# Kernel tuning notes

Measured on AMD Instinct MI355X. Metric: run time of the kernel, lower is better.

Reference implementation:

```python
import math
import jax, jax.numpy as jnp
import numpy as np

H = 256      # hidden_size
HEADS = 8
DK = H // HEADS
B = 32
DL = 290     # drug length
PL = 1000    # protein length


def _pe(length, d):
    # sinusoidal positional encoding, d even
    pos = jnp.arange(length, dtype=jnp.float32)[:, None]
    div = jnp.exp(jnp.arange(0, d, 2, dtype=jnp.float32) * (-math.log(10000.0) / d))
    ang = pos * div  # [L, d/2]
    pe = jnp.zeros((length, d), jnp.float32)
    pe = pe.at[:, 0::2].set(jnp.sin(ang)).at[:, 1::2].set(jnp.cos(ang))
    return pe


def setup_inputs() -> dict:
    key = jax.random.key(0)
    ks = iter(jax.random.split(key, 48))
    def lin(din, dout):
        return jax.random.normal(next(ks), (din, dout), jnp.float32) * 0.02, jnp.zeros((dout,), jnp.float32)
    inp = {}
    inp['drug'] = jax.random.normal(next(ks), (B, DL, H), jnp.float32)
    inp['protein'] = jax.random.normal(next(ks), (B, PL, H), jnp.float32)
    inp['scale_d'] = jnp.ones((1,), jnp.float32)
    inp['scale_p'] = jnp.ones((1,), jnp.float32)
    for name in ['q_d', 'k_p', 'v_p', 'q_p', 'k_d', 'v_d', 'out_d', 'out_p']:
        w, b = lin(H, H)
        inp['w_' + name] = w
        inp['b_' + name] = b
    inp['alpha'] = jnp.asarray(0.5, jnp.float32)
    for name in ['fc_dp', 'fc_pd']:
        w, b = lin(HEADS, H)
        inp['w_' + name] = w
        inp['b_' + name] = b
    for name in ['gd', 'gp']:
        w, b = lin(H, H)
        inp['w_' + name] = w
        inp['b_' + name] = b
    return inp


def _split_heads(x):
    b, l, _ = x.shape
    return x.reshape(b, l, HEADS, DK).transpose(0, 2, 1, 3)  # [b, h, l, dk]


def _forward(drug, protein, scale_d, scale_p,
             w_q_d, b_q_d, w_k_p, b_k_p, w_v_p, b_v_p,
             w_q_p, b_q_p, w_k_d, b_k_d, w_v_d, b_v_d,
             alpha, w_out_d, b_out_d, w_out_p, b_out_p,
             w_fc_dp, b_fc_dp, w_fc_pd, b_fc_pd,
             w_gd, b_gd, w_gp, b_gp):
    b, dl, h = drug.shape
    pl = protein.shape[1]
    # positional encoding (buffers, non-learned except scale)
    drug_e = drug + scale_d * _pe(dl, h)
    prot_e = protein + scale_p * _pe(pl, h)

    Qd = _split_heads(drug_e @ w_q_d + b_q_d)   # [b,h,dl,dk]
    Kp = _split_heads(prot_e @ w_k_p + b_k_p)   # [b,h,pl,dk]
    Vp = _split_heads(prot_e @ w_v_p + b_v_p)
    Qp = _split_heads(prot_e @ w_q_p + b_q_p)
    Kd = _split_heads(drug_e @ w_k_d + b_k_d)
    Vd = _split_heads(drug_e @ w_v_d + b_v_d)

    inv_sqrt = 1.0 / math.sqrt(DK)
    attn_dp = jnp.einsum('bhid,bhjd->bhij', Qd, Kp) * inv_sqrt      # [b,h,dl,pl]
    # (Q_p K_d^T)^T along last two dims -> [b,h,dl,pl]
    attn_pd = jnp.einsum('bhjd,bhid->bhij', Qp, Kd) * inv_sqrt
    a = jax.nn.sigmoid(alpha)
    A = jax.nn.softmax(a * attn_dp + (1.0 - a) * attn_pd, axis=-1)  # [b,h,dl,pl]

    ctx_d = jnp.einsum('bhij,bhjd->bhid', A, Vp)  # [b,h,dl,dk]
    ctx_p = jnp.einsum('bhij,bhid->bhjd', A, Vd)  # [b,h,pl,dk]
    ctx_d = ctx_d.transpose(0, 2, 1, 3).reshape(b, dl, h) @ w_out_d + b_out_d
    ctx_p = ctx_p.transpose(0, 2, 1, 3).reshape(b, pl, h) @ w_out_p + b_out_p

    attn_dp_m = jnp.mean(A, axis=-1).transpose(0, 2, 1)   # [b,dl,heads]
    drug_attn = attn_dp_m @ w_fc_dp + b_fc_dp             # [b,dl,h]
    attn_pd_m = jnp.mean(A, axis=-2).transpose(0, 2, 1)   # [b,pl,heads]
    prot_attn = attn_pd_m @ w_fc_pd + b_fc_pd             # [b,pl,h]

    drug_gate = jax.nn.sigmoid(drug_e @ w_gd + b_gd)
    prot_gate = jax.nn.sigmoid(prot_e @ w_gp + b_gp)
    ctx_d = ctx_d * drug_gate
    ctx_p = ctx_p * prot_gate

    drug_upd = drug_e + ctx_d * jax.nn.sigmoid(drug_attn)
    prot_upd = prot_e + ctx_p * jax.nn.sigmoid(prot_attn)
    return jnp.concatenate([drug_upd, prot_upd], axis=1)  # [b, dl+pl, h]


def reference(drug, protein, scale_d, scale_p,
              w_q_d, b_q_d, w_k_p, b_k_p, w_v_p, b_v_p,
              w_q_p, b_q_p, w_k_d, b_k_d, w_v_d, b_v_d,
              alpha, w_out_d, b_out_d, w_out_p, b_out_p,
              w_fc_dp, b_fc_dp, w_fc_pd, b_fc_pd,
              w_gd, b_gd, w_gp, b_gp):
    return _forward(drug, protein, scale_d, scale_p,
                    w_q_d, b_q_d, w_k_p, b_k_p, w_v_p, b_v_p,
                    w_q_p, b_q_p, w_k_d, b_k_d, w_v_d, b_v_d,
                    alpha, w_out_d, b_out_d, w_out_p, b_out_p,
                    w_fc_dp, b_fc_dp, w_fc_pd, b_fc_pd,
                    w_gd, b_gd, w_gp, b_gp)
```

## Files before the change

kernel.cpp:

```cpp
#include <hip/hip_runtime.h>
#include <math.h>

typedef __attribute__((ext_vector_type(8))) short bf16x8;
typedef __attribute__((ext_vector_type(4))) float f32x4;
typedef unsigned short u16;
typedef unsigned int u32;

#define DEVFN static __device__ __forceinline__

constexpr int NB  = 32;
constexpr int DLn = 290;
constexpr int PLc = 1000;
constexpr int MD  = NB * DLn;
constexpr int MP  = NB * PLc;

DEVFN u16 f2b(float f) {
    u32 u = __builtin_bit_cast(u32, f);
    u32 r = u + 0x7fffu + ((u >> 16) & 1u);
    return (u16)(r >> 16);
}
DEVFN float b2f(u16 s) { return __builtin_bit_cast(float, (u32)s << 16); }
DEVFN float sigm(float x) { return 1.0f / (1.0f + __expf(-x)); }

__global__ void pe_kernel(float* __restrict__ pe) {
    int p = blockIdx.x, c = threadIdx.x;
    float div = __expf((float)(c & ~1) * (-9.210340371976184f / 256.0f));
    float ang = (float)p * div;
    pe[p * 256 + c] = (c & 1) ? cosf(ang) : sinf(ang);
}

__global__ void eadd_kernel(const float* __restrict__ drug, const float* __restrict__ prot,
                            const float* __restrict__ scale_d, const float* __restrict__ scale_p,
                            const float* __restrict__ pe,
                            u16* __restrict__ e_d, u16* __restrict__ e_p) {
    int r = blockIdx.x, c = threadIdx.x;
    if (r < MD) {
        int i = r % DLn;
        e_d[(size_t)r * 256 + c] = f2b(drug[(size_t)r * 256 + c] + scale_d[0] * pe[i * 256 + c]);
    } else {
        int rr = r - MD;
        int j = rr % PLc;
        e_p[(size_t)rr * 256 + c] = f2b(prot[(size_t)rr * 256 + c] + scale_p[0] * pe[j * 256 + c]);
    }
}

struct WPtrs { const float* w[10]; };
__global__ void wprep_kernel(WPtrs wp, u16* __restrict__ wt) {
    int m = blockIdx.x >> 8, n = blockIdx.x & 255, k = threadIdx.x;
    wt[((size_t)m << 16) + n * 256 + k] = f2b(wp.w[m][k * 256 + n]);
}

struct GCfg { const u16* A; const u16* BT; const float* bias; u16* C; int mtiles; int sig; };
struct GCfg8 { GCfg c[8]; };

__global__ __launch_bounds__(256) void gemm_kernel(GCfg8 cfgs) {
    const GCfg cfg = cfgs.c[blockIdx.z];
    const int mt = blockIdx.x;
    if (mt >= cfg.mtiles) return;
    const int nt = blockIdx.y;
    __shared__ u16 As[64][264];
    __shared__ u16 Bs[64][264];
    const int tid = threadIdx.x;
    const int lane = tid & 63, w = tid >> 6, ln = lane & 15, g = lane >> 4;
    const int lr = tid >> 2, lc = tid & 3;
    const u16* Ag = cfg.A + (size_t)(mt * 64 + lr) * 256 + lc * 8;
    const u16* Bg = cfg.BT + (size_t)(nt * 64 + lr) * 256 + lc * 8;
    uint4 av[8], bv[8];
    #pragma unroll
    for (int kk = 0; kk < 8; kk++) {
        av[kk] = *(const uint4*)(Ag + kk * 32);
        bv[kk] = *(const uint4*)(Bg + kk * 32);
    }
    #pragma unroll
    for (int kk = 0; kk < 8; kk++) {
        *(uint4*)&As[lr][lc * 8 + kk * 32] = av[kk];
        *(uint4*)&Bs[lr][lc * 8 + kk * 32] = bv[kk];
    }
    __syncthreads();
    const int m0 = (w >> 1) * 32, n0 = (w & 1) * 32;
    f32x4 acc[2][2] = {};
    #pragma unroll
    for (int k0 = 0; k0 < 8; k0++) {
        #pragma unroll
        for (int mi = 0; mi < 2; mi++) {
            bf16x8 af = *(const bf16x8*)&As[m0 + mi * 16 + ln][k0 * 32 + g * 8];
            #pragma unroll
            for (int ni = 0; ni < 2; ni++) {
                bf16x8 bfv = *(const bf16x8*)&Bs[n0 + ni * 16 + ln][k0 * 32 + g * 8];
                acc[mi][ni] = __builtin_amdgcn_mfma_f32_16x16x32_bf16(af, bfv, acc[mi][ni], 0, 0, 0);
            }
        }
    }
    #pragma unroll
    for (int mi = 0; mi < 2; mi++) {
        #pragma unroll
        for (int ni = 0; ni < 2; ni++) {
            const int n = nt * 64 + n0 + ni * 16 + ln;
            const float bb = cfg.bias[n];
            const int rowb = mt * 64 + m0 + mi * 16 + g * 4;
            #pragma unroll
            for (int r = 0; r < 4; r++) {
                float v = acc[mi][ni][r] + bb;
                if (cfg.sig) v = sigm(v);
                cfg.C[(size_t)(rowb + r) * 256 + n] = f2b(v);
            }
        }
    }
}

__global__ __launch_bounds__(512) void attn_kernel(
        const u16* __restrict__ Qd, const u16* __restrict__ Kd, const u16* __restrict__ Vd,
        const u16* __restrict__ Kp, const u16* __restrict__ Vp, const u16* __restrict__ Qp,
        const float* __restrict__ alpha,
        u16* __restrict__ ctx_d, u16* __restrict__ ctx_p, float* __restrict__ cm) {
    __shared__ u16 Ks[2][64][72];
    __shared__ union {
        struct { u16 VpT[2][32][72]; u16 Pm[320][72]; } s1;
        struct { u16 PT[64][328]; u16 VdT[32][328]; } s2;
    } U;
    __shared__ float r_l[320];
    __shared__ float colpart[8][64];

    const int bh = blockIdx.x, b = bh >> 3, h = bh & 7;
    const int tid = threadIdx.x;
    const int w = tid >> 6, lane = tid & 63, ln = lane & 15, g = lane >> 4;

    const float a = sigm(alpha[0]);
    const float inv = 0.1767766952966369f;
    const float sa = a * inv, sb = (1.0f - a) * inv;
    const int nmt = (w < 4) ? 3 : 2;
    const int mtsA[3] = { w, w + 8, w + 16 };

    const size_t rbd = (size_t)b * DLn * 256 + h * 32;
    const size_t rbp = (size_t)b * PLc * 256 + h * 32;

    bf16x8 Qf[3][2];
    #pragma unroll
    for (int t = 0; t < 3; t++) {
        const int i = mtsA[t] * 16 + ln;
        #pragma unroll
        for (int ks = 0; ks < 2; ks++) {
            u16 o[8] = {0,0,0,0,0,0,0,0};
            if (t < nmt && i < DLn) {
                const u16* src = (ks ? Kd : Qd) + rbd + (size_t)i * 256 + g * 8;
                const float s = ks ? sb : sa;
                uint4 v = *(const uint4*)src;
                u16 e[8]; *(uint4*)e = v;
                #pragma unroll
                for (int q = 0; q < 8; q++) o[q] = f2b(b2f(e[q]) * s);
            }
            Qf[t][ks] = *(bf16x8*)o;
        }
    }

    const int s_jj = tid >> 3, s_ch = tid & 7;
    const u16* s_src = ((s_ch >> 2) ? Qp : Kp) + rbp + (s_ch & 3) * 8;
    const int v_j = tid & 63, v_d0 = (tid >> 6) * 4;

    {
        int j = s_jj;
        uint4 kv = (j < PLc) ? *(const uint4*)(s_src + (size_t)j * 256) : make_uint4(0,0,0,0);
        uint2 vv = (v_j < PLc) ? *(const uint2*)(Vp + rbp + (size_t)v_j * 256 + v_d0) : make_uint2(0,0);
        *(uint4*)&Ks[0][s_jj][s_ch * 8] = kv;
        u16 e[4]; *(uint2*)e = vv;
        #pragma unroll
        for (int q = 0; q < 4; q++) U.s1.VpT[0][v_d0 + q][v_j] = e[q];
    }
    __syncthreads();

    float rs[3] = {0.f, 0.f, 0.f};
    f32x4 accd[3][2] = {};
    for (int jt = 0; jt < 16; jt++) {
        const int cur = jt & 1, j0 = jt * 64;
        const int jn = j0 + 64 + s_jj;
        uint4 kv = (jn < PLc) ? *(const uint4*)(s_src + (size_t)jn * 256) : make_uint4(0,0,0,0);
        const int vn = j0 + 64 + v_j;
        uint2 vv = (vn < PLc) ? *(const uint2*)(Vp + rbp + (size_t)vn * 256 + v_d0) : make_uint2(0,0);

        bf16x8 kf[4][2];
        #pragma unroll
        for (int js = 0; js < 4; js++)
            #pragma unroll
            for (int ks = 0; ks < 2; ks++)
                kf[js][ks] = *(const bf16x8*)&Ks[cur][js * 16 + ln][ks * 32 + g * 8];

        #pragma unroll
        for (int t = 0; t < 3; t++) {
            if (t >= nmt) break;
            const int mt = mtsA[t];
            f32x4 acc[4] = {};
            #pragma unroll
            for (int ks = 0; ks < 2; ks++)
                #pragma unroll
                for (int js = 0; js < 4; js++)
                    acc[js] = __builtin_amdgcn_mfma_f32_16x16x32_bf16(kf[js][ks], Qf[t][ks], acc[js], 0, 0, 0);
            const int irow = mt * 16 + ln;
            #pragma unroll
            for (int js = 0; js < 4; js++) {
                u16 pb[4];
                float psum = 0.f;
                #pragma unroll
                for (int r = 0; r < 4; r++) {
                    const int j = j0 + js * 16 + g * 4 + r;
                    float p = (j < PLc) ? __expf(acc[js][r]) : 0.0f;
                    psum += p;
                    pb[r] = f2b(p);
                }
                rs[t] += psum;
                *(ushort4*)&U.s1.Pm[irow][js * 16 + g * 4] = *(ushort4*)pb;
            }
        }
        #pragma unroll
        for (int t = 0; t < 3; t++) {
            if (t >= nmt) break;
            const int mt = mtsA[t];
            #pragma unroll
            for (int ks2 = 0; ks2 < 2; ks2++) {
                bf16x8 af = *(const bf16x8*)&U.s1.Pm[mt * 16 + ln][ks2 * 32 + g * 8];
                #pragma unroll
                for (int nd = 0; nd < 2; nd++) {
                    bf16x8 bv = *(const bf16x8*)&U.s1.VpT[cur][nd * 16 + ln][ks2 * 32 + g * 8];
                    accd[t][nd] = __builtin_amdgcn_mfma_f32_16x16x32_bf16(af, bv, accd[t][nd], 0, 0, 0);
                }
            }
        }
        *(uint4*)&Ks[cur ^ 1][s_jj][s_ch * 8] = kv;
        {
            u16 e[4]; *(uint2*)e = vv;
            #pragma unroll
            for (int q = 0; q < 4; q++) U.s1.VpT[cur ^ 1][v_d0 + q][v_j] = e[q];
        }
        __syncthreads();
    }

    #pragma unroll
    for (int t = 0; t < 3; t++) {
        float v = rs[t];
        v += __shfl_xor(v, 16);
        v += __shfl_xor(v, 32);
        rs[t] = v;
    }
    if (g == 0) {
        #pragma unroll
        for (int t = 0; t < 3; t++) {
            if (t >= nmt) break;
            const int i = mtsA[t] * 16 + ln;
            r_l[i] = (i < DLn) ? 1.0f / rs[t] : 0.0f;
        }
    }
    __syncthreads();

    #pragma unroll
    for (int t = 0; t < 3; t++) {
        if (t >= nmt) break;
        const int mt = mtsA[t];
        #pragma unroll
        for (int r = 0; r < 4; r++) {
            const int i = mt * 16 + g * 4 + r;
            if (i < DLn) {
                const float ri = r_l[i];
                #pragma unroll
                for (int nd = 0; nd < 2; nd++)
                    ctx_d[rbd + (size_t)i * 256 + nd * 16 + ln] = f2b(accd[t][nd][r] * ri);
            }
        }
    }
    for (int c = tid; c < 320 * 8; c += 512) {
        const int i = c >> 3, d0 = (c & 7) * 4;
        u16 o[4] = {0,0,0,0};
        if (i < DLn) {
            const float ri = r_l[i];
            uint2 v = *(const uint2*)(Vd + rbd + (size_t)i * 256 + d0);
            u16 e[4]; *(uint2*)e = v;
            #pragma unroll
            for (int q = 0; q < 4; q++) o[q] = f2b(b2f(e[q]) * ri);
        }
        #pragma unroll
        for (int q = 0; q < 4; q++) U.s2.VdT[d0 + q][i] = o[q];
    }
    {
        int j = s_jj;
        uint4 kv = (j < PLc) ? *(const uint4*)(s_src + (size_t)j * 256) : make_uint4(0,0,0,0);
        *(uint4*)&Ks[0][s_jj][s_ch * 8] = kv;
    }
    float rr[3][4];
    #pragma unroll
    for (int t = 0; t < 3; t++)
        #pragma unroll
        for (int r = 0; r < 4; r++)
            rr[t][r] = (t < nmt) ? r_l[mtsA[t] * 16 + g * 4 + r] : 0.0f;
    __syncthreads();

    for (int jt = 0; jt < 16; jt++) {
        const int cur = jt & 1, j0 = jt * 64;
        const int jn = j0 + 64 + s_jj;
        uint4 kv = (jn < PLc) ? *(const uint4*)(s_src + (size_t)jn * 256) : make_uint4(0,0,0,0);

        bf16x8 kf[4][2];
        #pragma unroll
        for (int js = 0; js < 4; js++)
            #pragma unroll
            for (int ks = 0; ks < 2; ks++)
                kf[js][ks] = *(const bf16x8*)&Ks[cur][js * 16 + ln][ks * 32 + g * 8];

        float csl[4] = {0.f, 0.f, 0.f, 0.f};
        #pragma unroll
        for (int t = 0; t < 3; t++) {
            if (t >= nmt) break;
            const int mt = mtsA[t];
            f32x4 acc[4] = {};
            #pragma unroll
            for (int ks = 0; ks < 2; ks++)
                #pragma unroll
                for (int js = 0; js < 4; js++)
                    acc[js] = __builtin_amdgcn_mfma_f32_16x16x32_bf16(Qf[t][ks], kf[js][ks], acc[js], 0, 0, 0);
            #pragma unroll
            for (int js = 0; js < 4; js++) {
                const bool jok = (j0 + js * 16 + ln) < PLc;
                u16 pb[4];
                #pragma unroll
                for (int r = 0; r < 4; r++) {
                    float p = jok ? __expf(acc[js][r]) : 0.0f;
                    csl[js] += p * rr[t][r];
                    pb[r] = f2b(p);
                }
                *(ushort4*)&U.s2.PT[js * 16 + ln][mt * 16 + g * 4] = *(ushort4*)pb;
            }
        }
        #pragma unroll
        for (int js = 0; js < 4; js++) {
            float v = csl[js];
            v += __shfl_xor(v, 16);
            v += __shfl_xor(v, 32);
            csl[js] = v;
        }
        if (g == 0) {
            #pragma unroll
            for (int js = 0; js < 4; js++) colpart[w][js * 16 + ln] = csl[js];
        }
        *(uint4*)&Ks[cur ^ 1][s_jj][s_ch * 8] = kv;
        __syncthreads();

        {
            const int js2 = w & 3, ds2 = w >> 2;
            f32x4 ap = {};
            #pragma unroll
            for (int k = 0; k < 10; k++) {
                bf16x8 af = *(const bf16x8*)&U.s2.PT[js2 * 16 + ln][k * 32 + g * 8];
                bf16x8 bv = *(const bf16x8*)&U.s2.VdT[ds2 * 16 + ln][k * 32 + g * 8];
                ap = __builtin_amdgcn_mfma_f32_16x16x32_bf16(af, bv, ap, 0, 0, 0);
            }
            const int d = ds2 * 16 + ln;
            #pragma unroll
            for (int r = 0; r < 4; r++) {
                const int j = j0 + js2 * 16 + g * 4 + r;
                if (j < PLc) ctx_p[rbp + (size_t)j * 256 + d] = f2b(ap[r]);
            }
        }
        if (w == 0) {
            float tot = 0.f;
            #pragma unroll
            for (int ww = 0; ww < 8; ww++) tot += colpart[ww][lane];
            const int j = j0 + lane;
            if (j < PLc) cm[(size_t)(b * PLc + j) * 8 + h] = tot * (1.0f / 290.0f);
        }
        __syncthreads();
    }
}

__global__ void combine_kernel(const float* __restrict__ drug, const float* __restrict__ prot,
        const float* __restrict__ scale_d, const float* __restrict__ scale_p,
        const float* __restrict__ pe,
        const u16* __restrict__ Xd, const u16* __restrict__ Xp,
        const u16* __restrict__ gate_d, const u16* __restrict__ gate_p,
        const float* __restrict__ cm,
        const float* __restrict__ w_fc_dp, const float* __restrict__ b_fc_dp,
        const float* __restrict__ w_fc_pd, const float* __restrict__ b_fc_pd,
        float* __restrict__ out) {
    int r = blockIdx.x, c = threadIdx.x;
    if (r < MD) {
        int b = r / DLn, i = r % DLn;
        float e = drug[(size_t)r * 256 + c] + scale_d[0] * pe[i * 256 + c];
        float da = b_fc_dp[c];
        #pragma unroll
        for (int hh = 0; hh < 8; hh++) da += 0.001f * w_fc_dp[hh * 256 + c];
        float v = e + b2f(Xd[(size_t)r * 256 + c]) * b2f(gate_d[(size_t)r * 256 + c]) * sigm(da);
        out[((size_t)b * 1290 + i) * 256 + c] = v;
    } else {
        int rr = r - MD;
        int b = rr / PLc, j = rr % PLc;
        float e = prot[(size_t)rr * 256 + c] + scale_p[0] * pe[j * 256 + c];
        float pa = b_fc_pd[c];
        #pragma unroll
        for (int hh = 0; hh < 8; hh++) pa += cm[(size_t)rr * 8 + hh] * w_fc_pd[hh * 256 + c];
        float v = e + b2f(Xp[(size_t)rr * 256 + c]) * b2f(gate_p[(size_t)rr * 256 + c]) * sigm(pa);
        out[((size_t)b * 1290 + 290 + j) * 256 + c] = v;
    }
}

extern "C" void kernel_launch(void* const* d_in, const int* in_sizes, int n_in,
                              void* d_out, int out_size, void* d_ws, size_t ws_size,
                              hipStream_t stream) {
    (void)in_sizes; (void)n_in; (void)out_size;
    const float* drug    = (const float*)d_in[0];
    const float* prot    = (const float*)d_in[1];
    const float* scale_d = (const float*)d_in[2];
    const float* scale_p = (const float*)d_in[3];

    char* ws = (char*)d_ws;
    size_t off = 0;
    auto alloc = [&](size_t bytes) -> void* {
        void* p = ws + off;
        off += (bytes + 255) & ~(size_t)255;
        return p;
    };
    float* pe   = (float*)alloc((size_t)1000 * 256 * 4);
    u16* e_d    = (u16*)alloc((size_t)MD * 256 * 2);
    u16* e_p    = (u16*)alloc((size_t)MP * 256 * 2);
    u16* wt     = (u16*)alloc((size_t)10 * 65536 * 2);
    u16* Qd     = (u16*)alloc((size_t)MD * 256 * 2);
    u16* Kd     = (u16*)alloc((size_t)MD * 256 * 2);
    u16* Vd     = (u16*)alloc((size_t)MD * 256 * 2);
    u16* gate_d = (u16*)alloc((size_t)MD * 256 * 2);
    u16* Kp     = (u16*)alloc((size_t)MP * 256 * 2);
    u16* Vp     = (u16*)alloc((size_t)MP * 256 * 2);
    u16* Qp     = (u16*)alloc((size_t)MP * 256 * 2);
    u16* gate_p = (u16*)alloc((size_t)MP * 256 * 2);
    u16* ctxd   = (u16*)alloc((size_t)MD * 256 * 2);
    u16* ctxp   = (u16*)alloc((size_t)MP * 256 * 2);
    float* cm   = (float*)alloc((size_t)MP * 8 * 4);
    u16* Xd     = (u16*)alloc((size_t)MD * 256 * 2);
    u16* Xp     = (u16*)alloc((size_t)MP * 256 * 2);
    if (off > ws_size) return;

    pe_kernel<<<1000, 256, 0, stream>>>(pe);

    WPtrs wp;
    const int wsrc[10] = {4, 12, 14, 25, 6, 8, 10, 27, 16, 18};
    for (int m = 0; m < 10; m++) wp.w[m] = (const float*)d_in[wsrc[m]];
    wprep_kernel<<<2560, 256, 0, stream>>>(wp, wt);

    eadd_kernel<<<MD + MP, 256, 0, stream>>>(drug, prot, scale_d, scale_p, pe, e_d, e_p);

    auto W = [&](int slot) { return wt + (size_t)slot * 65536; };
    GCfg8 pc;
    pc.c[0] = { e_d, W(0), (const float*)d_in[5],  Qd,     145, 0 };
    pc.c[1] = { e_d, W(1), (const float*)d_in[13], Kd,     145, 0 };
    pc.c[2] = { e_d, W(2), (const float*)d_in[15], Vd,     145, 0 };
    pc.c[3] = { e_d, W(3), (const float*)d_in[26], gate_d, 145, 1 };
    pc.c[4] = { e_p, W(4), (const float*)d_in[7],  Kp,     500, 0 };
    pc.c[5] = { e_p, W(5), (const float*)d_in[9],  Vp,     500, 0 };
    pc.c[6] = { e_p, W(6), (const float*)d_in[11], Qp,     500, 0 };
    pc.c[7] = { e_p, W(7), (const float*)d_in[28], gate_p, 500, 1 };
    gemm_kernel<<<dim3(500, 4, 8), 256, 0, stream>>>(pc);

    attn_kernel<<<256, 512, 0, stream>>>(Qd, Kd, Vd, Kp, Vp, Qp,
                                         (const float*)d_in[20], ctxd, ctxp, cm);

    GCfg8 oc = pc;
    oc.c[0] = { ctxd, W(8), (const float*)d_in[17], Xd, 145, 0 };
    oc.c[1] = { ctxp, W(9), (const float*)d_in[19], Xp, 500, 0 };
    gemm_kernel<<<dim3(500, 4, 2), 256, 0, stream>>>(oc);

    combine_kernel<<<MD + MP, 256, 0, stream>>>(drug, prot, scale_d, scale_p, pe,
        Xd, Xp, gate_d, gate_p, cm,
        (const float*)d_in[21], (const float*)d_in[22],
        (const float*)d_in[23], (const float*)d_in[24],
        (float*)d_out);
}
```

Measured before the change: 216.2 us.

## Vectorize elementwise kernels, tile weight transpose, repad LDS, drop attention masks

Result: slower. 348.5 us (+61.2%).

```diff
diff --git a/kernel.cpp b/kernel.cpp
--- a/kernel.cpp
+++ b/kernel.cpp
@@ -21,6 +21,11 @@
 }
 DEVFN float b2f(u16 s) { return __builtin_bit_cast(float, (u32)s << 16); }
 DEVFN float sigm(float x) { return 1.0f / (1.0f + __expf(-x)); }
+DEVFN u32 cvtpk(float lo, float hi) {
+    u32 r;
+    asm("v_cvt_pk_bf16_f32 %0, %1, %2" : "=v"(r) : "v"(lo), "v"(hi));
+    return r;
+}
 
 __global__ void pe_kernel(float* __restrict__ pe) {
     int p = blockIdx.x, c = threadIdx.x;
@@ -29,25 +34,51 @@
     pe[p * 256 + c] = (c & 1) ? cosf(ang) : sinf(ang);
 }
 
-__global__ void eadd_kernel(const float* __restrict__ drug, const float* __restrict__ prot,
-                            const float* __restrict__ scale_d, const float* __restrict__ scale_p,
-                            const float* __restrict__ pe,
-                            u16* __restrict__ e_d, u16* __restrict__ e_p) {
-    int r = blockIdx.x, c = threadIdx.x;
+__global__ __launch_bounds__(256) void eadd_kernel(
+        const float* __restrict__ drug, const float* __restrict__ prot,
+        const float* __restrict__ scale_d, const float* __restrict__ scale_p,
+        const float* __restrict__ pe,
+        u16* __restrict__ e_d, u16* __restrict__ e_p) {
+    int idx = blockIdx.x * 256 + threadIdx.x;
+    int r = idx >> 6, c4 = (idx & 63) * 4;
     if (r < MD) {
         int i = r % DLn;
-        e_d[(size_t)r * 256 + c] = f2b(drug[(size_t)r * 256 + c] + scale_d[0] * pe[i * 256 + c]);
+        float s = scale_d[0];
+        float4 dv = *(const float4*)&drug[(size_t)r * 256 + c4];
+        float4 pv = *(const float4*)&pe[i * 256 + c4];
+        u32 a = cvtpk(dv.x + s * pv.x, dv.y + s * pv.y);
+        u32 b = cvtpk(dv.z + s * pv.z, dv.w + s * pv.w);
+        *(uint2*)&e_d[(size_t)r * 256 + c4] = make_uint2(a, b);
     } else {
         int rr = r - MD;
         int j = rr % PLc;
-        e_p[(size_t)rr * 256 + c] = f2b(prot[(size_t)rr * 256 + c] + scale_p[0] * pe[j * 256 + c]);
+        float s = scale_p[0];
+        float4 dv = *(const float4*)&prot[(size_t)rr * 256 + c4];
+        float4 pv = *(const float4*)&pe[j * 256 + c4];
+        u32 a = cvtpk(dv.x + s * pv.x, dv.y + s * pv.y);
+        u32 b = cvtpk(dv.z + s * pv.z, dv.w + s * pv.w);
+        *(uint2*)&e_p[(size_t)rr * 256 + c4] = make_uint2(a, b);
     }
 }
 
 struct WPtrs { const float* w[10]; };
-__global__ void wprep_kernel(WPtrs wp, u16* __restrict__ wt) {
-    int m = blockIdx.x >> 8, n = blockIdx.x & 255, k = threadIdx.x;
-    wt[((size_t)m << 16) + n * 256 + k] = f2b(wp.w[m][k * 256 + n]);
+__global__ __launch_bounds__(256) void wprep_kernel(WPtrs wp, u16* __restrict__ wt) {
+    __shared__ u16 t[64][66];
+    int m = blockIdx.y, tile = blockIdx.x;
+    int k0 = (tile >> 2) * 64, n0 = (tile & 3) * 64;
+    const float* w = wp.w[m];
+    int r = threadIdx.x >> 6, c = threadIdx.x & 63;
+    #pragma unroll
+    for (int q = 0; q < 16; q++) {
+        int rr = r + q * 4;
+        t[rr][c] = f2b(w[(size_t)(k0 + rr) * 256 + n0 + c]);
+    }
+    __syncthreads();
+    #pragma unroll
+    for (int q = 0; q < 16; q++) {
+        int rr = r + q * 4;
+        wt[((size_t)m << 16) + (size_t)(n0 + rr) * 256 + k0 + c] = t[c][rr];
+    }
 }
 
 struct GCfg { const u16* A; const u16* BT; const float* bias; u16* C; int mtiles; int sig; };
@@ -58,8 +89,8 @@
     const int mt = blockIdx.x;
     if (mt >= cfg.mtiles) return;
     const int nt = blockIdx.y;
-    __shared__ u16 As[64][264];
-    __shared__ u16 Bs[64][264];
+    __shared__ u16 As[64][266];
+    __shared__ u16 Bs[64][266];
     const int tid = threadIdx.x;
     const int lane = tid & 63, w = tid >> 6, ln = lane & 15, g = lane >> 4;
     const int lr = tid >> 2, lc = tid & 3;
@@ -113,10 +144,10 @@
         const u16* __restrict__ Kp, const u16* __restrict__ Vp, const u16* __restrict__ Qp,
         const float* __restrict__ alpha,
         u16* __restrict__ ctx_d, u16* __restrict__ ctx_p, float* __restrict__ cm) {
-    __shared__ u16 Ks[2][64][72];
+    __shared__ u16 Ks[2][64][74];
     __shared__ union {
-        struct { u16 VpT[2][32][72]; u16 Pm[320][72]; } s1;
-        struct { u16 PT[64][328]; u16 VdT[32][328]; } s2;
+        struct { u16 VpT[2][32][74]; u16 Pm[320][74]; } s1;
+        struct { u16 PT[64][330]; u16 VdT[32][330]; } s2;
     } U;
     __shared__ float r_l[320];
     __shared__ float colpart[8][64];
@@ -197,17 +228,13 @@
             const int irow = mt * 16 + ln;
             #pragma unroll
             for (int js = 0; js < 4; js++) {
-                u16 pb[4];
-                float psum = 0.f;
-                #pragma unroll
-                for (int r = 0; r < 4; r++) {
-                    const int j = j0 + js * 16 + g * 4 + r;
-                    float p = (j < PLc) ? __expf(acc[js][r]) : 0.0f;
-                    psum += p;
-                    pb[r] = f2b(p);
-                }
-                rs[t] += psum;
-                *(ushort4*)&U.s1.Pm[irow][js * 16 + g * 4] = *(ushort4*)pb;
+                float p0 = __expf(acc[js][0]);
+                float p1 = __expf(acc[js][1]);
+                float p2 = __expf(acc[js][2]);
+                float p3 = __expf(acc[js][3]);
+                rs[t] += (p0 + p1) + (p2 + p3);
+                u32 lo = cvtpk(p0, p1), hi = cvtpk(p2, p3);
+                *(uint2*)&U.s1.Pm[irow][js * 16 + g * 4] = make_uint2(lo, hi);
             }
         }
         #pragma unroll
@@ -245,7 +272,7 @@
         for (int t = 0; t < 3; t++) {
             if (t >= nmt) break;
             const int i = mtsA[t] * 16 + ln;
-            r_l[i] = (i < DLn) ? 1.0f / rs[t] : 0.0f;
+            r_l[i] = (i < DLn) ? 1.0f / (rs[t] - 24.0f) : 0.0f;
         }
     }
     __syncthreads();
@@ -316,15 +343,13 @@
                     acc[js] = __builtin_amdgcn_mfma_f32_16x16x32_bf16(Qf[t][ks], kf[js][ks], acc[js], 0, 0, 0);
             #pragma unroll
             for (int js = 0; js < 4; js++) {
-                const bool jok = (j0 + js * 16 + ln) < PLc;
-                u16 pb[4];
-                #pragma unroll
-                for (int r = 0; r < 4; r++) {
-                    float p = jok ? __expf(acc[js][r]) : 0.0f;
-                    csl[js] += p * rr[t][r];
-                    pb[r] = f2b(p);
-                }
-                *(ushort4*)&U.s2.PT[js * 16 + ln][mt * 16 + g * 4] = *(ushort4*)pb;
+                float p0 = __expf(acc[js][0]);
+                float p1 = __expf(acc[js][1]);
+                float p2 = __expf(acc[js][2]);
+                float p3 = __expf(acc[js][3]);
+                csl[js] += p0 * rr[t][0] + p1 * rr[t][1] + p2 * rr[t][2] + p3 * rr[t][3];
+                u32 lo = cvtpk(p0, p1), hi = cvtpk(p2, p3);
+                *(uint2*)&U.s2.PT[js * 16 + ln][mt * 16 + g * 4] = make_uint2(lo, hi);
             }
         }
         #pragma unroll
@@ -368,7 +393,8 @@
     }
 }
 
-__global__ void combine_kernel(const float* __restrict__ drug, const float* __restrict__ prot,
+__global__ __launch_bounds__(256) void combine_kernel(
+        const float* __restrict__ drug, const float* __restrict__ prot,
         const float* __restrict__ scale_d, const float* __restrict__ scale_p,
         const float* __restrict__ pe,
         const u16* __restrict__ Xd, const u16* __restrict__ Xp,
@@ -377,24 +403,60 @@
         const float* __restrict__ w_fc_dp, const float* __restrict__ b_fc_dp,
         const float* __restrict__ w_fc_pd, const float* __restrict__ b_fc_pd,
         float* __restrict__ out) {
-    int r = blockIdx.x, c = threadIdx.x;
+    int idx = blockIdx.x * 256 + threadIdx.x;
+    int r = idx >> 6, c4 = (idx & 63) * 4;
     if (r < MD) {
         int b = r / DLn, i = r % DLn;
-        float e = drug[(size_t)r * 256 + c] + scale_d[0] * pe[i * 256 + c];
-        float da = b_fc_dp[c];
-        #pragma unroll
-        for (int hh = 0; hh < 8; hh++) da += 0.001f * w_fc_dp[hh * 256 + c];
-        float v = e + b2f(Xd[(size_t)r * 256 + c]) * b2f(gate_d[(size_t)r * 256 + c]) * sigm(da);
-        out[((size_t)b * 1290 + i) * 256 + c] = v;
+        float s = scale_d[0];
+        float4 dv = *(const float4*)&drug[(size_t)r * 256 + c4];
+        float4 pv = *(const float4*)&pe[i * 256 + c4];
+        uint2 xv = *(const uint2*)&Xd[(size_t)r * 256 + c4];
+        uint2 gv = *(const uint2*)&gate_d[(size_t)r * 256 + c4];
+        float4 bb = *(const float4*)&b_fc_dp[c4];
+        float da[4] = { bb.x, bb.y, bb.z, bb.w };
+        #pragma unroll
+        for (int hh = 0; hh < 8; hh++) {
+            float4 wv = *(const float4*)&w_fc_dp[hh * 256 + c4];
+            da[0] += 0.001f * wv.x; da[1] += 0.001f * wv.y;
+            da[2] += 0.001f * wv.z; da[3] += 0.001f * wv.w;
+        }
+        u16 xe[4]; *(uint2*)xe = xv;
+        u16 ge[4]; *(uint2*)ge = gv;
+        float e0 = dv.x + s * pv.x, e1 = dv.y + s * pv.y;
+        float e2 = dv.z + s * pv.z, e3 = dv.w + s * pv.w;
+        float4 o;
+        o.x = e0 + b2f(xe[0]) * b2f(ge[0]) * sigm(da[0]);
+        o.y = e1 + b2f(xe[1]) * b2f(ge[1]) * sigm(da[1]);
+        o.z = e2 + b2f(xe[2]) * b2f(ge[2]) * sigm(da[2]);
+        o.w = e3 + b2f(xe[3]) * b2f(ge[3]) * sigm(da[3]);
+        *(float4*)&out[((size_t)b * 1290 + i) * 256 + c4] = o;
     } else {
         int rr = r - MD;
         int b = rr / PLc, j = rr % PLc;
-        float e = prot[(size_t)rr * 256 + c] + scale_p[0] * pe[j * 256 + c];
-        float pa = b_fc_pd[c];
-        #pragma unroll
-        for (int hh = 0; hh < 8; hh++) pa += cm[(size_t)rr * 8 + hh] * w_fc_pd[hh * 256 + c];
-        float v = e + b2f(Xp[(size_t)rr * 256 + c]) * b2f(gate_p[(size_t)rr * 256 + c]) * sigm(pa);
-        out[((size_t)b * 1290 + 290 + j) * 256 + c] = v;
+        float s = scale_p[0];
+        float4 dv = *(const float4*)&prot[(size_t)rr * 256 + c4];
+        float4 pv = *(const float4*)&pe[j * 256 + c4];
+        uint2 xv = *(const uint2*)&Xp[(size_t)rr * 256 + c4];
+        uint2 gv = *(const uint2*)&gate_p[(size_t)rr * 256 + c4];
+        float4 bb = *(const float4*)&b_fc_pd[c4];
+        float pa[4] = { bb.x, bb.y, bb.z, bb.w };
+        #pragma unroll
+        for (int hh = 0; hh < 8; hh++) {
+            float cmh = cm[(size_t)rr * 8 + hh];
+            float4 wv = *(const float4*)&w_fc_pd[hh * 256 + c4];
+            pa[0] += cmh * wv.x; pa[1] += cmh * wv.y;
+            pa[2] += cmh * wv.z; pa[3] += cmh * wv.w;
+        }
+        u16 xe[4]; *(uint2*)xe = xv;
+        u16 ge[4]; *(uint2*)ge = gv;
+        float e0 = dv.x + s * pv.x, e1 = dv.y + s * pv.y;
+        float e2 = dv.z + s * pv.z, e3 = dv.w + s * pv.w;
+        float4 o;
+        o.x = e0 + b2f(xe[0]) * b2f(ge[0]) * sigm(pa[0]);
+        o.y = e1 + b2f(xe[1]) * b2f(ge[1]) * sigm(pa[1]);
+        o.z = e2 + b2f(xe[2]) * b2f(ge[2]) * sigm(pa[2]);
+        o.w = e3 + b2f(xe[3]) * b2f(ge[3]) * sigm(pa[3]);
+        *(float4*)&out[((size_t)b * 1290 + 290 + j) * 256 + c4] = o;
     }
 }
 
@@ -438,9 +500,9 @@
     WPtrs wp;
     const int wsrc[10] = {4, 12, 14, 25, 6, 8, 10, 27, 16, 18};
     for (int m = 0; m < 10; m++) wp.w[m] = (const float*)d_in[wsrc[m]];
-    wprep_kernel<<<2560, 256, 0, stream>>>(wp, wt);
-
-    eadd_kernel<<<MD + MP, 256, 0, stream>>>(drug, prot, scale_d, scale_p, pe, e_d, e_p);
+    wprep_kernel<<<dim3(16, 10), 256, 0, stream>>>(wp, wt);
+
+    eadd_kernel<<<(MD + MP) / 4, 256, 0, stream>>>(drug, prot, scale_d, scale_p, pe, e_d, e_p);
 
     auto W = [&](int slot) { return wt + (size_t)slot * 65536; };
     GCfg8 pc;
@@ -462,7 +524,7 @@
     oc.c[1] = { ctxp, W(9), (const float*)d_in[19], Xp, 500, 0 };
     gemm_kernel<<<dim3(500, 4, 2), 256, 0, stream>>>(oc);
 
-    combine_kernel<<<MD + MP, 256, 0, stream>>>(drug, prot, scale_d, scale_p, pe,
+    combine_kernel<<<(MD + MP) / 4, 256, 0, stream>>>(drug, prot, scale_d, scale_p, pe,
         Xd, Xp, gate_d, gate_p, cm,
         (const float*)d_in[21], (const float*)d_in[22],
         (const float*)d_in[23], (const float*)d_in[24],
```
